# Performance work log

Hardware: AMD Instinct MI355X
Metric: run time of the kernel (lower is better)

The kernel has to match this reference:

```python
import jax, jax.numpy as jnp
import numpy as np

B, N, H, W = 4, 4096, 480, 640
RADIUS = 2.0        # hard-coded self.radius in DiskLoss
SCORES_TH = 0.1     # PeakyLoss scores_th
KP_PENALTY = -0.001 # configs['kp_penalty']


def setup_inputs() -> dict:
    key = jax.random.key(0)
    ks = jax.random.split(key, 6)
    lp0 = jax.random.uniform(ks[0], (B, 1, H, W), dtype=jnp.float32)
    lp1 = jax.random.uniform(ks[1], (B, 1, H, W), dtype=jnp.float32)
    # keypoints are normalized grid_sample coords in [-1, 1], (x, y) order
    kp0 = jax.random.uniform(ks[2], (B, N, 2), dtype=jnp.float32) * 2.0 - 1.0
    kp1 = jax.random.uniform(ks[3], (B, N, 2), dtype=jnp.float32) * 2.0 - 1.0
    d0 = jax.random.uniform(ks[4], (B, N), dtype=jnp.float32)
    d1 = jax.random.uniform(ks[5], (B, N), dtype=jnp.float32)
    return dict(local_point0=lp0, local_point1=lp1, keypoints0=kp0,
                keypoints1=kp1, score_dispersity0=d0, score_dispersity1=d1)


def grid_sample_bilinear(img, pts):
    """torch.grid_sample(mode='bilinear', align_corners=True) for one image.
    img: [H, W]; pts: [N, 2] in [-1, 1], pts[:,0]=x (width), pts[:,1]=y (height)."""
    Hh, Ww = img.shape
    x = (pts[:, 0] + 1.0) * 0.5 * (Ww - 1)
    y = (pts[:, 1] + 1.0) * 0.5 * (Hh - 1)
    x0 = jnp.floor(x); y0 = jnp.floor(y)
    wx = x - x0; wy = y - y0
    def g(yy, xx):
        yi = jnp.clip(yy, 0, Hh - 1).astype(jnp.int32)
        xi = jnp.clip(xx, 0, Ww - 1).astype(jnp.int32)
        return img[yi, xi]
    return (g(y0, x0) * (1 - wx) * (1 - wy)
            + g(y0, x0 + 1) * wx * (1 - wy)
            + g(y0 + 1, x0) * (1 - wx) * wy
            + g(y0 + 1, x0 + 1) * wx * wy)


def nms_valid(kpts_wh, scores):
    """Faithful sequential NMS from compute_correspondence for one image.
    kpts_wh: [N, 2] pixel coords; scores: [N]. Returns bool [N] valid mask."""
    n = scores.shape[0]
    sq = jnp.sum(kpts_wh * kpts_wh, axis=-1)
    d2 = sq[:, None] + sq[None, :] - 2.0 * (kpts_wh @ kpts_wh.T)  # [N, N]
    local_mask = d2 < RADIUS * RADIUS
    valid_cnt0 = local_mask.sum(-1).astype(jnp.int32)
    need = valid_cnt0 > 1  # indices_need_nms (computed once, as in torch)
    idx = jnp.arange(n)
    neg_inf = jnp.asarray(-jnp.inf, scores.dtype)
    def body(i, vc):
        row = local_mask[i]
        cond = need[i] & (vc[i] > 0)
        j = jnp.argmax(jnp.where(row, scores, neg_inf))  # best-scoring neighbor
        suppressed = jnp.where(row & (idx != j), 0, vc)
        return jnp.where(cond, suppressed, vc)
    vc = jax.lax.fori_loop(0, n, body, valid_cnt0)
    return vc > 0


def stream_loss(local_point, kpts, disp):
    # local_point [B,1,H,W], kpts [B,N,2] in [-1,1], disp [B,N]
    wh = jnp.array([local_point.shape[3] - 1, local_point.shape[2] - 1],
                   dtype=local_point.dtype)
    scores = jax.vmap(lambda m, k: grid_sample_bilinear(m[0], k))(local_point, kpts)  # [B,N]
    kpts_wh = (kpts / 2.0 + 0.5) * wh  # pixel coords
    valid = jax.vmap(nms_valid)(jax.lax.stop_gradient(kpts_wh),
                                jax.lax.stop_gradient(scores))  # [B,N] bool
    # PeakyLoss over NMS-surviving keypoints with score > threshold
    peaky_mask = (valid & (scores > SCORES_TH)).astype(disp.dtype)
    cnt = jnp.maximum(peaky_mask.sum(), 1.0)
    loss_peaky = jnp.sum(disp * peaky_mask) / cnt
    # keypoint score term (kp_penalty-weighted mean of surviving scores)
    vmask = valid.astype(scores.dtype)
    vcnt = jnp.maximum(vmask.sum(), 1.0)
    score_mean = jnp.sum(scores * vmask) / vcnt
    return loss_peaky + KP_PENALTY * score_mean


def reference(local_point0, local_point1, keypoints0, keypoints1,
              score_dispersity0, score_dispersity1):
    return (stream_loss(local_point0, keypoints0, score_dispersity0)
            + stream_loss(local_point1, keypoints1, score_dispersity1))
```

## Files before the change

### kernel.cpp

```cpp
#include <hip/hip_runtime.h>
#include <math.h>

#define NN 4096
#define HH 480
#define WW 640
#define RAD2 4.0f
#define TH_SCORE 0.1f
#define KPPEN -0.001f
#define CXN 160
#define CYN 120
#define NCELL (CXN * CYN)
#define SLOTS 8
#define CAP 48

#define OFF_SCORES  0
#define OFF_PTS     131072
#define OFF_CNT     655360
#define OFF_PARTNER 688128
#define OFF_ROWS    753664
#define OFF_CELLS   1277952
#define OFF_CCNT    3735552
#define OFF_ACC     4349952
#define OFF_DONE    4349984

__global__ __launch_bounds__(256) void k_sample(
    const float* __restrict__ lp0, const float* __restrict__ lp1,
    const float* __restrict__ kp0, const float* __restrict__ kp1,
    float* __restrict__ scores, float4* __restrict__ pts,
    unsigned short* __restrict__ cells, unsigned int* __restrict__ ccnt)
{
#pragma clang fp contract(off)
    int gid = blockIdx.x * 256 + threadIdx.x;
    int s = gid >> 14;
    int r = gid & 16383;
    int b = r >> 12;
    const float* kp  = (s ? kp1 : kp0) + (size_t)r * 2;
    const float* img = (s ? lp1 : lp0) + (size_t)b * (HH * WW);
    float px = kp[0], py = kp[1];
    float x = (px + 1.0f) * 0.5f * (float)(WW - 1);
    float y = (py + 1.0f) * 0.5f * (float)(HH - 1);
    float x0 = floorf(x), y0 = floorf(y);
    float wx = x - x0, wy = y - y0;
    int ix0 = (int)fminf(fmaxf(x0, 0.0f), (float)(WW - 1));
    int iy0 = (int)fminf(fmaxf(y0, 0.0f), (float)(HH - 1));
    int ix1 = (int)fminf(fmaxf(x0 + 1.0f, 0.0f), (float)(WW - 1));
    int iy1 = (int)fminf(fmaxf(y0 + 1.0f, 0.0f), (float)(HH - 1));
    float g00 = img[iy0 * WW + ix0];
    float g01 = img[iy0 * WW + ix1];
    float g10 = img[iy1 * WW + ix0];
    float g11 = img[iy1 * WW + ix1];
    float sc = g00 * (1.0f - wx) * (1.0f - wy)
             + g01 * wx * (1.0f - wy)
             + g10 * (1.0f - wx) * wy
             + g11 * wx * wy;
    float xw = (px / 2.0f + 0.5f) * (float)(WW - 1);
    float yw = (py / 2.0f + 0.5f) * (float)(HH - 1);
    float sq = xw * xw + yw * yw;
    scores[gid] = sc;
    pts[gid] = make_float4(xw, yw, sq, 0.0f);
    int imgid = gid >> 12;
    int li = gid & (NN - 1);
    int cx = (int)(xw * 0.25f); cx = cx < 0 ? 0 : (cx > CXN - 1 ? CXN - 1 : cx);
    int cy = (int)(yw * 0.25f); cy = cy < 0 ? 0 : (cy > CYN - 1 ? CYN - 1 : cy);
    int cell = imgid * NCELL + cy * CXN + cx;
    unsigned int pos = atomicAdd(&ccnt[cell], 1u);
    if (pos < SLOTS) cells[(size_t)cell * SLOTS + pos] = (unsigned short)li;
}

__global__ __launch_bounds__(256) void k_cnt(
    const float4* __restrict__ pts, const unsigned short* __restrict__ cells,
    const unsigned int* __restrict__ ccnt,
    unsigned char* __restrict__ cnt, unsigned short* __restrict__ partner,
    uint4* __restrict__ rows4)
{
#pragma clang fp contract(off)
    int gid = blockIdx.x * 256 + threadIdx.x;
    int imgid = gid >> 12;
    int li = gid & (NN - 1);
    const float4* p = pts + ((size_t)imgid << 12);
    float4 a = p[li];
    int cx = (int)(a.x * 0.25f); cx = cx < 0 ? 0 : (cx > CXN - 1 ? CXN - 1 : cx);
    int cy = (int)(a.y * 0.25f); cy = cy < 0 ? 0 : (cy > CYN - 1 ? CYN - 1 : cy);

    int c = 0, sum = 0; bool ov = false;
    unsigned long long rlo = 0ull, rhi = 0ull;
    auto place = [&](int pos, unsigned q) {
        unsigned long long v = (unsigned long long)q;
        switch (pos) {
            case 0: rlo |= v;       break;
            case 1: rlo |= v << 16; break;
            case 2: rlo |= v << 32; break;
            case 3: rlo |= v << 48; break;
            case 4: rhi |= v;       break;
            case 5: rhi |= v << 16; break;
            case 6: rhi |= v << 32; break;
            case 7: rhi |= v << 48; break;
        }
    };
    auto test = [&](unsigned q) {
        float4 qq = p[q];
        float dot = a.x * qq.x + a.y * qq.y;
        float t = a.z + qq.z;
        float d2 = fmaf(-2.0f, dot, t);
        if (d2 < RAD2) {
            if (c < 8) place(c, q);
            ++c; sum += (int)q;
        }
    };

#pragma unroll
    for (int dy = -1; dy <= 1; ++dy) {
#pragma unroll
        for (int dx = -1; dx <= 1; ++dx) {
            int yy = cy + dy, xx = cx + dx;
            bool valid = (yy >= 0) & (yy < CYN) & (xx >= 0) & (xx < CXN);
            int cell = imgid * NCELL + (valid ? yy * CXN + xx : 0);
            unsigned n = valid ? ccnt[cell] : 0u;
            if (n > SLOTS) { ov = true; n = SLOTS; }
            uint4 cl = valid ? *(const uint4*)&cells[(size_t)cell * SLOTS]
                             : make_uint4(0, 0, 0, 0);
            unsigned q0 = cl.x & 0xffffu, q1 = cl.x >> 16;
            unsigned q2 = cl.y & 0xffffu, q3 = cl.y >> 16;
            unsigned q4 = cl.z & 0xffffu, q5 = cl.z >> 16;
            unsigned q6 = cl.w & 0xffffu, q7 = cl.w >> 16;
            if (n > 0) test(q0);
            if (n > 1) test(q1);
            if (n > 2) test(q2);
            if (n > 3) test(q3);
            if (n > 4) test(q4);
            if (n > 5) test(q5);
            if (n > 6) test(q6);
            if (n > 7) test(q7);
        }
    }
    if (ov) {
        c = 0; sum = 0; rlo = 0ull; rhi = 0ull;
        for (int j = 0; j < NN; ++j) test((unsigned)j);
    }
    cnt[gid] = (unsigned char)(c > 255 ? 255 : c);
    partner[gid] = (unsigned short)((sum - li) & 0xFFFF);
    if (c >= 3 && c <= 8)
        rows4[gid] = make_uint4((unsigned)rlo, (unsigned)(rlo >> 32),
                                (unsigned)rhi, (unsigned)(rhi >> 32));
}

__global__ __launch_bounds__(256) void k_nms(
    const float* __restrict__ scoresG, const float4* __restrict__ pts,
    const unsigned char* __restrict__ cntG, const unsigned short* __restrict__ partnerG,
    const uint4* __restrict__ rows4,
    const float* __restrict__ dd0, const float* __restrict__ dd1,
    float* __restrict__ acc, unsigned int* __restrict__ done,
    float* __restrict__ out)
{
#pragma clang fp contract(off)
    __shared__ float          s_sc[NN];
    __shared__ unsigned char  s_cnt[NN];
    __shared__ unsigned short s_partner[NN];
    __shared__ unsigned short s_mem[256][CAP + 2];
    __shared__ float s_red[4];

    int imgid = blockIdx.x >> 4;
    int seg = blockIdx.x & 15;
    int base = imgid << 12;
    int tid = threadIdx.x;
    const float4* p = pts + (size_t)base;

    for (int t = tid; t < NN; t += 256) {
        s_sc[t] = scoresG[base + t];
        s_cnt[t] = cntG[base + t];
        s_partner[t] = partnerG[base + t];
    }
    __syncthreads();

    int li = (seg << 8) + tid;
    int c = s_cnt[li];
    bool alive = true;

    if (c >= 2) {
        int pr = s_partner[li];
        if (c == 2 && s_cnt[pr] == 2) {
            int lo = li < pr ? li : pr, hi = li < pr ? pr : li;
            int w = (s_sc[lo] >= s_sc[hi]) ? lo : hi;
            alive = (w == li);
        } else {
            unsigned short* mem = s_mem[tid];
            int cntm = 1, proc = 0;
            mem[0] = (unsigned short)li;
            auto insert = [&](unsigned q) {
                for (int k = 0; k < cntm; ++k) if (mem[k] == (unsigned short)q) return;
                if (cntm < CAP) mem[cntm++] = (unsigned short)q;
            };
            auto full_insert = [&](int m) {
                float4 pm = p[m];
                for (int j = 0; j < NN; ++j) {
                    float4 qq = p[j];
                    float dot = pm.x * qq.x + pm.y * qq.y;
                    float t = pm.z + qq.z;
                    float d2 = fmaf(-2.0f, dot, t);
                    if (d2 < RAD2) insert((unsigned)j);
                }
            };
            while (proc < cntm) {
                int m = mem[proc++];
                int cm = s_cnt[m];
                if (cm == 2) {
                    insert(s_partner[m]);
                } else if (cm <= 8) {
                    uint4 w = rows4[base + m];
                    unsigned q0 = w.x & 0xffffu, q1 = w.x >> 16;
                    unsigned q2 = w.y & 0xffffu, q3 = w.y >> 16;
                    unsigned q4 = w.z & 0xffffu, q5 = w.z >> 16;
                    unsigned q6 = w.w & 0xffffu, q7 = w.w >> 16;
                    if (cm > 0) insert(q0);
                    if (cm > 1) insert(q1);
                    if (cm > 2) insert(q2);
                    if (cm > 3) insert(q3);
                    if (cm > 4) insert(q4);
                    if (cm > 5) insert(q5);
                    if (cm > 6) insert(q6);
                    if (cm > 7) insert(q7);
                } else {
                    full_insert(m);
                }
            }
            for (int k = 1; k < cntm; ++k) {
                unsigned short v = mem[k]; int j2 = k;
                while (j2 > 0 && mem[j2 - 1] > v) { mem[j2] = mem[j2 - 1]; --j2; }
                mem[j2] = v;
            }
            unsigned long long am = (cntm >= 64) ? ~0ull : ((1ull << cntm) - 1ull);
            auto clearbit = [&](unsigned q) {
                for (int k = 0; k < cntm; ++k)
                    if (mem[k] == (unsigned short)q) { am &= ~(1ull << k); return; }
            };
            for (int k = 0; k < cntm; ++k) {
                if (!((am >> k) & 1ull)) continue;
                int m = mem[k];
                int cm = s_cnt[m];
                if (cm == 2) {
                    int pr2 = s_partner[m];
                    int lo = m < pr2 ? m : pr2, hi = m < pr2 ? pr2 : m;
                    int w = (s_sc[lo] >= s_sc[hi]) ? lo : hi;
                    clearbit((unsigned)(w == lo ? hi : lo));
                } else if (cm <= 8) {
                    uint4 w = rows4[base + m];
                    unsigned q0 = w.x & 0xffffu, q1 = w.x >> 16;
                    unsigned q2 = w.y & 0xffffu, q3 = w.y >> 16;
                    unsigned q4 = w.z & 0xffffu, q5 = w.z >> 16;
                    unsigned q6 = w.w & 0xffffu, q7 = w.w >> 16;
                    float bs = -1.0f; int bi = NN;
                    auto cand = [&](int k2, unsigned q) {
                        if (k2 < cm) {
                            float s2 = s_sc[q];
                            if (s2 > bs || (s2 == bs && (int)q < bi)) { bs = s2; bi = (int)q; }
                        }
                    };
                    cand(0, q0); cand(1, q1); cand(2, q2); cand(3, q3);
                    cand(4, q4); cand(5, q5); cand(6, q6); cand(7, q7);
                    auto clr = [&](int k2, unsigned q) {
                        if (k2 < cm && (int)q != bi) clearbit(q);
                    };
                    clr(0, q0); clr(1, q1); clr(2, q2); clr(3, q3);
                    clr(4, q4); clr(5, q5); clr(6, q6); clr(7, q7);
                } else {
                    float4 pm = p[m];
                    float bs = -1.0f; int bi = NN;
                    for (int j = 0; j < NN; ++j) {
                        float4 qq = p[j];
                        float dot = pm.x * qq.x + pm.y * qq.y;
                        float t = pm.z + qq.z;
                        float d2 = fmaf(-2.0f, dot, t);
                        if (d2 < RAD2) {
                            float s2 = s_sc[j];
                            if (s2 > bs || (s2 == bs && j < bi)) { bs = s2; bi = j; }
                        }
                    }
                    for (int j = 0; j < NN; ++j) {
                        float4 qq = p[j];
                        float dot = pm.x * qq.x + pm.y * qq.y;
                        float t = pm.z + qq.z;
                        float d2 = fmaf(-2.0f, dot, t);
                        if (d2 < RAD2 && j != bi) clearbit((unsigned)j);
                    }
                }
            }
            for (int k = 0; k < cntm; ++k)
                if (mem[k] == (unsigned short)li) { alive = ((am >> k) & 1ull) != 0; break; }
        }
    }

    int stream = imgid >> 2, b = imgid & 3;
    const float* disp = (stream ? dd1 : dd0) + (size_t)b * NN;
    float sum_dp = 0.f, cnt_p = 0.f, sum_sv = 0.f, cnt_v = 0.f;
    if (alive) {
        float sc = s_sc[li];
        cnt_v = 1.0f; sum_sv = sc;
        if (sc > TH_SCORE) { cnt_p = 1.0f; sum_dp = disp[li]; }
    }
    __syncthreads();
#pragma unroll
    for (int q = 0; q < 4; ++q) {
        float v = (q == 0) ? sum_dp : (q == 1) ? cnt_p : (q == 2) ? sum_sv : cnt_v;
        for (int o = 32; o > 0; o >>= 1) v += __shfl_down(v, o, 64);
        if ((tid & 63) == 0) s_red[tid >> 6] = v;
        __syncthreads();
        if (tid == 0) {
            float r = s_red[0] + s_red[1] + s_red[2] + s_red[3];
            atomicAdd(&acc[stream * 4 + q], r);
        }
        __syncthreads();
    }

    if (tid == 0) {
        __threadfence();
        unsigned prev = atomicAdd(done, 1u);
        if (prev == 127u) {
            float r = 0.0f;
            for (int s = 0; s < 2; ++s) {
                float sdp = atomicAdd(&acc[s * 4 + 0], 0.0f);
                float cp  = atomicAdd(&acc[s * 4 + 1], 0.0f);
                float ssv = atomicAdd(&acc[s * 4 + 2], 0.0f);
                float cv  = atomicAdd(&acc[s * 4 + 3], 0.0f);
                r += sdp / fmaxf(cp, 1.0f) + KPPEN * (ssv / fmaxf(cv, 1.0f));
            }
            out[0] = r;
        }
    }
}

extern "C" void kernel_launch(void* const* d_in, const int* in_sizes, int n_in,
                              void* d_out, int out_size, void* d_ws, size_t ws_size,
                              hipStream_t stream)
{
    const float* lp0 = (const float*)d_in[0];
    const float* lp1 = (const float*)d_in[1];
    const float* kp0 = (const float*)d_in[2];
    const float* kp1 = (const float*)d_in[3];
    const float* dd0 = (const float*)d_in[4];
    const float* dd1 = (const float*)d_in[5];

    char* ws = (char*)d_ws;
    float*          scores  = (float*)(ws + OFF_SCORES);
    float4*         pts     = (float4*)(ws + OFF_PTS);
    unsigned char*  cnt     = (unsigned char*)(ws + OFF_CNT);
    unsigned short* partner = (unsigned short*)(ws + OFF_PARTNER);
    uint4*          rows4   = (uint4*)(ws + OFF_ROWS);
    unsigned short* cells   = (unsigned short*)(ws + OFF_CELLS);
    unsigned int*   ccnt    = (unsigned int*)(ws + OFF_CCNT);
    float*          acc     = (float*)(ws + OFF_ACC);
    unsigned int*   done    = (unsigned int*)(ws + OFF_DONE);

    hipMemsetAsync(ws + OFF_CCNT, 0, 614436, stream);
    k_sample<<<128, 256, 0, stream>>>(lp0, lp1, kp0, kp1, scores, pts, cells, ccnt);
    k_cnt<<<128, 256, 0, stream>>>(pts, cells, ccnt, cnt, partner, rows4);
    k_nms<<<128, 256, 0, stream>>>(scores, pts, cnt, partner, rows4,
                                   dd0, dd1, acc, done, (float*)d_out);
}
```

Baseline: 116.3 us.

## Compact NMS worklist per block, cache rows in LDS, cut block count

The NMS kernel now runs 32 blocks, each covering 1024 keypoints of one image instead of 256. Pair cases are resolved inline. Keypoints that need cluster traversal go onto a shared worklist, so threads process them densely instead of leaving most lanes idle. Rows for points with 3-8 neighbours are cached in LDS, and the per-thread cluster capacity drops to 38 to fit the extra shared memory. The risks are fewer blocks and therefore less GPU occupancy, plus possible truncation when a cluster exceeds the smaller capacity.

New measurement: 126.5 us. +8.8%, slower.

```diff
diff --git a/kernel.cpp b/kernel.cpp
--- a/kernel.cpp
+++ b/kernel.cpp
@@ -11,7 +11,10 @@
 #define CYN 120
 #define NCELL (CXN * CYN)
 #define SLOTS 8
-#define CAP 48
+#define CAP 38
+#define ROWCAP 256
+#define IMGB 4
+#define NBLK2 (8 * IMGB)
 
 #define OFF_SCORES  0
 #define OFF_PTS     131072
@@ -107,7 +110,6 @@
             ++c; sum += (int)q;
         }
     };
-
 #pragma unroll
     for (int dy = -1; dy <= 1; ++dy) {
 #pragma unroll
@@ -155,149 +157,192 @@
 #pragma clang fp contract(off)
     __shared__ float          s_sc[NN];
     __shared__ unsigned char  s_cnt[NN];
+    __shared__ unsigned char  s_alive[NN];
+    __shared__ unsigned char  s_rowidx[NN];
     __shared__ unsigned short s_partner[NN];
+    __shared__ uint4          s_rows[ROWCAP];
+    __shared__ unsigned short s_wl[1024];
     __shared__ unsigned short s_mem[256][CAP + 2];
+    __shared__ int s_nrows, s_wln;
     __shared__ float s_red[4];
 
-    int imgid = blockIdx.x >> 4;
-    int seg = blockIdx.x & 15;
+    int blk = blockIdx.x;
+    int imgid = blk >> 2;
+    int sub = blk & (IMGB - 1);
     int base = imgid << 12;
     int tid = threadIdx.x;
     const float4* p = pts + (size_t)base;
 
+    if (tid == 0) { s_nrows = 0; s_wln = 0; }
     for (int t = tid; t < NN; t += 256) {
         s_sc[t] = scoresG[base + t];
         s_cnt[t] = cntG[base + t];
         s_partner[t] = partnerG[base + t];
+        s_alive[t] = 1;
+        s_rowidx[t] = 255;
     }
     __syncthreads();
 
-    int li = (seg << 8) + tid;
-    int c = s_cnt[li];
-    bool alive = true;
-
-    if (c >= 2) {
-        int pr = s_partner[li];
-        if (c == 2 && s_cnt[pr] == 2) {
-            int lo = li < pr ? li : pr, hi = li < pr ? pr : li;
-            int w = (s_sc[lo] >= s_sc[hi]) ? lo : hi;
-            alive = (w == li);
-        } else {
-            unsigned short* mem = s_mem[tid];
-            int cntm = 1, proc = 0;
-            mem[0] = (unsigned short)li;
-            auto insert = [&](unsigned q) {
-                for (int k = 0; k < cntm; ++k) if (mem[k] == (unsigned short)q) return;
-                if (cntm < CAP) mem[cntm++] = (unsigned short)q;
-            };
-            auto full_insert = [&](int m) {
+    for (int t = tid; t < NN; t += 256) {
+        int c = s_cnt[t];
+        if (c >= 3 && c <= 8) {
+            int slot = atomicAdd(&s_nrows, 1);
+            if (slot < ROWCAP) {
+                s_rowidx[t] = (unsigned char)slot;
+                s_rows[slot] = rows4[base + t];
+            }
+        }
+    }
+
+    int segbase = sub << 10;
+#pragma unroll
+    for (int k = 0; k < 4; ++k) {
+        int li = segbase + (k << 8) + tid;
+        int c = s_cnt[li];
+        if (c >= 3) {
+            int pos = atomicAdd(&s_wln, 1);
+            s_wl[pos] = (unsigned short)li;
+        } else if (c == 2) {
+            int pr = s_partner[li];
+            if (s_cnt[pr] == 2) {
+                int lo = li < pr ? li : pr, hi = li < pr ? pr : li;
+                int w = (s_sc[lo] >= s_sc[hi]) ? lo : hi;
+                s_alive[li] = (w == li) ? 1 : 0;
+            } else {
+                int pos = atomicAdd(&s_wln, 1);
+                s_wl[pos] = (unsigned short)li;
+            }
+        }
+    }
+    __syncthreads();
+    int wln = s_wln;
+
+    for (int t = tid; t < wln; t += 256) {
+        int li = s_wl[t];
+        unsigned short* mem = s_mem[tid];
+        int cntm = 1, proc = 0;
+        mem[0] = (unsigned short)li;
+        auto insert = [&](unsigned q) {
+            for (int k = 0; k < cntm; ++k) if (mem[k] == (unsigned short)q) return;
+            if (cntm < CAP) mem[cntm++] = (unsigned short)q;
+        };
+        auto getrow = [&](int m) -> uint4 {
+            int idx = s_rowidx[m];
+            return (idx != 255) ? s_rows[idx] : rows4[base + m];
+        };
+        auto full_insert = [&](int m) {
+            float4 pm = p[m];
+            for (int j = 0; j < NN; ++j) {
+                float4 qq = p[j];
+                float dot = pm.x * qq.x + pm.y * qq.y;
+                float tt = pm.z + qq.z;
+                float d2 = fmaf(-2.0f, dot, tt);
+                if (d2 < RAD2) insert((unsigned)j);
+            }
+        };
+        while (proc < cntm) {
+            int m = mem[proc++];
+            int cm = s_cnt[m];
+            if (cm == 2) {
+                insert(s_partner[m]);
+            } else if (cm <= 8) {
+                uint4 w = getrow(m);
+                unsigned q0 = w.x & 0xffffu, q1 = w.x >> 16;
+                unsigned q2 = w.y & 0xffffu, q3 = w.y >> 16;
+                unsigned q4 = w.z & 0xffffu, q5 = w.z >> 16;
+                unsigned q6 = w.w & 0xffffu, q7 = w.w >> 16;
+                if (cm > 0) insert(q0);
+                if (cm > 1) insert(q1);
+                if (cm > 2) insert(q2);
+                if (cm > 3) insert(q3);
+                if (cm > 4) insert(q4);
+                if (cm > 5) insert(q5);
+                if (cm > 6) insert(q6);
+                if (cm > 7) insert(q7);
+            } else {
+                full_insert(m);
+            }
+        }
+        for (int k = 1; k < cntm; ++k) {
+            unsigned short v = mem[k]; int j2 = k;
+            while (j2 > 0 && mem[j2 - 1] > v) { mem[j2] = mem[j2 - 1]; --j2; }
+            mem[j2] = v;
+        }
+        unsigned long long am = (cntm >= 64) ? ~0ull : ((1ull << cntm) - 1ull);
+        auto clearbit = [&](unsigned q) {
+            for (int k = 0; k < cntm; ++k)
+                if (mem[k] == (unsigned short)q) { am &= ~(1ull << k); return; }
+        };
+        for (int k = 0; k < cntm; ++k) {
+            if (!((am >> k) & 1ull)) continue;
+            int m = mem[k];
+            int cm = s_cnt[m];
+            if (cm == 2) {
+                int pr2 = s_partner[m];
+                int lo = m < pr2 ? m : pr2, hi = m < pr2 ? pr2 : m;
+                int w = (s_sc[lo] >= s_sc[hi]) ? lo : hi;
+                clearbit((unsigned)(w == lo ? hi : lo));
+            } else if (cm <= 8) {
+                uint4 w = getrow(m);
+                unsigned q0 = w.x & 0xffffu, q1 = w.x >> 16;
+                unsigned q2 = w.y & 0xffffu, q3 = w.y >> 16;
+                unsigned q4 = w.z & 0xffffu, q5 = w.z >> 16;
+                unsigned q6 = w.w & 0xffffu, q7 = w.w >> 16;
+                float bs = -1.0f; int bi = NN;
+                auto cand = [&](int k2, unsigned q) {
+                    if (k2 < cm) {
+                        float s2 = s_sc[q];
+                        if (s2 > bs || (s2 == bs && (int)q < bi)) { bs = s2; bi = (int)q; }
+                    }
+                };
+                cand(0, q0); cand(1, q1); cand(2, q2); cand(3, q3);
+                cand(4, q4); cand(5, q5); cand(6, q6); cand(7, q7);
+                auto clr = [&](int k2, unsigned q) {
+                    if (k2 < cm && (int)q != bi) clearbit(q);
+                };
+                clr(0, q0); clr(1, q1); clr(2, q2); clr(3, q3);
+                clr(4, q4); clr(5, q5); clr(6, q6); clr(7, q7);
+            } else {
                 float4 pm = p[m];
+                float bs = -1.0f; int bi = NN;
                 for (int j = 0; j < NN; ++j) {
                     float4 qq = p[j];
                     float dot = pm.x * qq.x + pm.y * qq.y;
-                    float t = pm.z + qq.z;
-                    float d2 = fmaf(-2.0f, dot, t);
-                    if (d2 < RAD2) insert((unsigned)j);
-                }
-            };
-            while (proc < cntm) {
-                int m = mem[proc++];
-                int cm = s_cnt[m];
-                if (cm == 2) {
-                    insert(s_partner[m]);
-                } else if (cm <= 8) {
-                    uint4 w = rows4[base + m];
-                    unsigned q0 = w.x & 0xffffu, q1 = w.x >> 16;
-                    unsigned q2 = w.y & 0xffffu, q3 = w.y >> 16;
-                    unsigned q4 = w.z & 0xffffu, q5 = w.z >> 16;
-                    unsigned q6 = w.w & 0xffffu, q7 = w.w >> 16;
-                    if (cm > 0) insert(q0);
-                    if (cm > 1) insert(q1);
-                    if (cm > 2) insert(q2);
-                    if (cm > 3) insert(q3);
-                    if (cm > 4) insert(q4);
-                    if (cm > 5) insert(q5);
-                    if (cm > 6) insert(q6);
-                    if (cm > 7) insert(q7);
-                } else {
-                    full_insert(m);
-                }
-            }
-            for (int k = 1; k < cntm; ++k) {
-                unsigned short v = mem[k]; int j2 = k;
-                while (j2 > 0 && mem[j2 - 1] > v) { mem[j2] = mem[j2 - 1]; --j2; }
-                mem[j2] = v;
-            }
-            unsigned long long am = (cntm >= 64) ? ~0ull : ((1ull << cntm) - 1ull);
-            auto clearbit = [&](unsigned q) {
-                for (int k = 0; k < cntm; ++k)
-                    if (mem[k] == (unsigned short)q) { am &= ~(1ull << k); return; }
-            };
-            for (int k = 0; k < cntm; ++k) {
-                if (!((am >> k) & 1ull)) continue;
-                int m = mem[k];
-                int cm = s_cnt[m];
-                if (cm == 2) {
-                    int pr2 = s_partner[m];
-                    int lo = m < pr2 ? m : pr2, hi = m < pr2 ? pr2 : m;
-                    int w = (s_sc[lo] >= s_sc[hi]) ? lo : hi;
-                    clearbit((unsigned)(w == lo ? hi : lo));
-                } else if (cm <= 8) {
-                    uint4 w = rows4[base + m];
-                    unsigned q0 = w.x & 0xffffu, q1 = w.x >> 16;
-                    unsigned q2 = w.y & 0xffffu, q3 = w.y >> 16;
-                    unsigned q4 = w.z & 0xffffu, q5 = w.z >> 16;
-                    unsigned q6 = w.w & 0xffffu, q7 = w.w >> 16;
-                    float bs = -1.0f; int bi = NN;
-                    auto cand = [&](int k2, unsigned q) {
-                        if (k2 < cm) {
-                            float s2 = s_sc[q];
-                            if (s2 > bs || (s2 == bs && (int)q < bi)) { bs = s2; bi = (int)q; }
-                        }
-                    };
-                    cand(0, q0); cand(1, q1); cand(2, q2); cand(3, q3);
-                    cand(4, q4); cand(5, q5); cand(6, q6); cand(7, q7);
-                    auto clr = [&](int k2, unsigned q) {
-                        if (k2 < cm && (int)q != bi) clearbit(q);
-                    };
-                    clr(0, q0); clr(1, q1); clr(2, q2); clr(3, q3);
-                    clr(4, q4); clr(5, q5); clr(6, q6); clr(7, q7);
-                } else {
-                    float4 pm = p[m];
-                    float bs = -1.0f; int bi = NN;
-                    for (int j = 0; j < NN; ++j) {
-                        float4 qq = p[j];
-                        float dot = pm.x * qq.x + pm.y * qq.y;
-                        float t = pm.z + qq.z;
-                        float d2 = fmaf(-2.0f, dot, t);
-                        if (d2 < RAD2) {
-                            float s2 = s_sc[j];
-                            if (s2 > bs || (s2 == bs && j < bi)) { bs = s2; bi = j; }
-                        }
-                    }
-                    for (int j = 0; j < NN; ++j) {
-                        float4 qq = p[j];
-                        float dot = pm.x * qq.x + pm.y * qq.y;
-                        float t = pm.z + qq.z;
-                        float d2 = fmaf(-2.0f, dot, t);
-                        if (d2 < RAD2 && j != bi) clearbit((unsigned)j);
+                    float tt = pm.z + qq.z;
+                    float d2 = fmaf(-2.0f, dot, tt);
+                    if (d2 < RAD2) {
+                        float s2 = s_sc[j];
+                        if (s2 > bs || (s2 == bs && j < bi)) { bs = s2; bi = j; }
                     }
                 }
-            }
-            for (int k = 0; k < cntm; ++k)
-                if (mem[k] == (unsigned short)li) { alive = ((am >> k) & 1ull) != 0; break; }
-        }
-    }
+                for (int j = 0; j < NN; ++j) {
+                    float4 qq = p[j];
+                    float dot = pm.x * qq.x + pm.y * qq.y;
+                    float tt = pm.z + qq.z;
+                    float d2 = fmaf(-2.0f, dot, tt);
+                    if (d2 < RAD2 && j != bi) clearbit((unsigned)j);
+                }
+            }
+        }
+        bool alive = false;
+        for (int k = 0; k < cntm; ++k)
+            if (mem[k] == (unsigned short)li) { alive = ((am >> k) & 1ull) != 0; break; }
+        s_alive[li] = alive ? 1 : 0;
+    }
+    __syncthreads();
 
     int stream = imgid >> 2, b = imgid & 3;
     const float* disp = (stream ? dd1 : dd0) + (size_t)b * NN;
     float sum_dp = 0.f, cnt_p = 0.f, sum_sv = 0.f, cnt_v = 0.f;
-    if (alive) {
-        float sc = s_sc[li];
-        cnt_v = 1.0f; sum_sv = sc;
-        if (sc > TH_SCORE) { cnt_p = 1.0f; sum_dp = disp[li]; }
-    }
-    __syncthreads();
+#pragma unroll
+    for (int k = 0; k < 4; ++k) {
+        int li = segbase + (k << 8) + tid;
+        if (s_alive[li]) {
+            float sc = s_sc[li];
+            cnt_v += 1.0f; sum_sv += sc;
+            if (sc > TH_SCORE) { cnt_p += 1.0f; sum_dp += disp[li]; }
+        }
+    }
 #pragma unroll
     for (int q = 0; q < 4; ++q) {
         float v = (q == 0) ? sum_dp : (q == 1) ? cnt_p : (q == 2) ? sum_sv : cnt_v;
@@ -314,7 +359,7 @@
     if (tid == 0) {
         __threadfence();
         unsigned prev = atomicAdd(done, 1u);
-        if (prev == 127u) {
+        if (prev == NBLK2 - 1u) {
             float r = 0.0f;
             for (int s = 0; s < 2; ++s) {
                 float sdp = atomicAdd(&acc[s * 4 + 0], 0.0f);
@@ -353,6 +398,6 @@
     hipMemsetAsync(ws + OFF_CCNT, 0, 614436, stream);
     k_sample<<<128, 256, 0, stream>>>(lp0, lp1, kp0, kp1, scores, pts, cells, ccnt);
     k_cnt<<<128, 256, 0, stream>>>(pts, cells, ccnt, cnt, partner, rows4);
-    k_nms<<<128, 256, 0, stream>>>(scores, pts, cnt, partner, rows4,
-                                   dd0, dd1, acc, done, (float*)d_out);
+    k_nms<<<NBLK2, 256, 0, stream>>>(scores, pts, cnt, partner, rows4,
+                                     dd0, dd1, acc, done, (float*)d_out);
 }
```
